# Optimization experiments

Hardware: AMD Instinct MI355X
Metric: run time of the kernel (lower is better)

Reference implementation:

```python
import jax, jax.numpy as jnp
import numpy as np

B, S, D = 4, 512, 512
H = 8
HD = D // H  # 64
F = 5  # num membership functions
EPS = 1e-8


def setup_inputs() -> dict:
    key = jax.random.key(0)
    ks = jax.random.split(key, 8)
    inp = {
        "x": jax.random.normal(ks[0], (B, S, D), jnp.float32),
        # linear projections (stored so that y = x @ W + b)
        "Wq": jax.random.normal(ks[1], (D, D), jnp.float32) / np.sqrt(D),
        "bq": jnp.zeros((D,), jnp.float32),
        "Wk": jax.random.normal(ks[2], (D, D), jnp.float32) / np.sqrt(D),
        "bk": jnp.zeros((D,), jnp.float32),
        "Wv": jax.random.normal(ks[3], (D, D), jnp.float32) / np.sqrt(D),
        "bv": jnp.zeros((D,), jnp.float32),
        "Wo": jax.random.normal(ks[4], (D, D), jnp.float32) / np.sqrt(D),
        "bo": jnp.zeros((D,), jnp.float32),
        # Gaussian membership params (init per nn.Parameter defaults)
        "g_centers": jax.random.normal(ks[5], (F, HD), jnp.float32),
        "g_sigmas": jnp.ones((F, HD), jnp.float32),
        "g_weights": jnp.ones((F,), jnp.float32),
        # learnable t-norm mixing logits
        "tnorm_weights": jnp.ones((3,), jnp.float32),
    }
    return inp


def _gaussian_membership(z, centers, sigmas, weights):
    # z: [B,H,S,HD] -> membership [B,H,S,F]
    nd = (z[..., None, :] - centers) / (sigmas + EPS)  # [B,H,S,F,HD]
    # prod_k exp(-0.5 nd_k^2) == exp(sum_k -0.5 nd_k^2)
    mem = jnp.exp(jnp.sum(-0.5 * nd * nd, axis=-1))  # [B,H,S,F]
    return mem * weights


def reference(x, Wq, bq, Wk, bk, Wv, bv, Wo, bo,
              g_centers, g_sigmas, g_weights, tnorm_weights):
    b, s, d = x.shape
    q = (x @ Wq + bq).reshape(b, s, H, HD).transpose(0, 2, 1, 3)  # [B,H,S,HD]
    k = (x @ Wk + bk).reshape(b, s, H, HD).transpose(0, 2, 1, 3)
    v = (x @ Wv + bv).reshape(b, s, H, HD).transpose(0, 2, 1, 3)

    qm = _gaussian_membership(q, g_centers, g_sigmas, g_weights)  # [B,H,S,F]
    km = _gaussian_membership(k, g_centers, g_sigmas, g_weights)  # [B,H,S,F]

    w = jax.nn.softmax(tnorm_weights)
    # product t-norm summed over F is a plain contraction
    prod_term = jnp.einsum('bhif,bhjf->bhij', qm, km)
    qe = qm[:, :, :, None, :]  # [B,H,S,1,F]
    ke = km[:, :, None, :, :]  # [B,H,1,S,F]
    min_term = jnp.sum(jnp.minimum(qe, ke), axis=-1)           # [B,H,S,S]
    luk_term = jnp.sum(jnp.maximum(qe + ke - 1.0, 0.0), axis=-1)
    scores = w[0] * prod_term + w[1] * min_term + w[2] * luk_term
    attn = jax.nn.softmax(scores, axis=-1)  # [B,H,S,S]

    out = jnp.einsum('bhij,bhjd->bhid', attn, v)  # [B,H,S,HD]
    out = out.transpose(0, 2, 1, 3).reshape(b, s, d)
    out = out @ Wo + bo  # dropout is identity in eval mode
    return out, attn
```

## Files before the change

kernel.cpp:

```cpp
#include <hip/hip_runtime.h>
#include <hip/hip_bf16.h>

#define B_  4
#define S_  512
#define D_  512
#define H_  8
#define HD_ 64
#define F_  5
#define NROW (B_*S_)
#define BHS  (B_*H_*S_)
#define EPS_ 1e-8f

typedef __attribute__((ext_vector_type(8))) short bf16x8;
typedef __attribute__((ext_vector_type(4))) float f32x4;

static __device__ __forceinline__ short f2bf(float f) {
    __hip_bfloat16 h = __float2bfloat16(f);
    return *reinterpret_cast<short*>(&h);
}

#define GLOAD16(ldsp, gp) \
    __builtin_amdgcn_global_load_lds( \
        (const __attribute__((address_space(1))) unsigned int*)(gp), \
        (__attribute__((address_space(3))) unsigned int*)(ldsp), 16, 0, 0)

__global__ __launch_bounds__(256) void convert_fused(
    const float* __restrict__ x,
    const float* __restrict__ Wq, const float* __restrict__ Wk,
    const float* __restrict__ Wv, const float* __restrict__ Wo,
    short* __restrict__ xb, short* __restrict__ WqkvT, short* __restrict__ WoT)
{
    const int bid = blockIdx.x;
    if (bid < 1024) {
        int i = bid * 256 + threadIdx.x;
        float4 f = reinterpret_cast<const float4*>(x)[i];
        short4 o;
        o.x = f2bf(f.x); o.y = f2bf(f.y); o.z = f2bf(f.z); o.w = f2bf(f.w);
        reinterpret_cast<short4*>(xb)[i] = o;
        return;
    }
    const int wb = bid - 1024;
    const int widx = wb >> 6;
    const int tile = wb & 63;
    const int k0 = (tile >> 3) * 64, n0 = (tile & 7) * 64;
    const float* __restrict__ src = widx==0?Wq:(widx==1?Wk:(widx==2?Wv:Wo));
    short* __restrict__ dst = (widx < 3) ? WqkvT : WoT;
    const int drow0 = (widx < 3) ? widx * 512 : 0;

    __shared__ short T[64][72];
    const int t = threadIdx.x;
    const int r = t >> 2, qq = t & 3;
#pragma unroll
    for (int i = 0; i < 4; ++i) {
        float4 f = *reinterpret_cast<const float4*>(&src[(k0+r)*D_ + n0 + qq*16 + i*4]);
        T[r][qq*16+i*4+0] = f2bf(f.x);
        T[r][qq*16+i*4+1] = f2bf(f.y);
        T[r][qq*16+i*4+2] = f2bf(f.z);
        T[r][qq*16+i*4+3] = f2bf(f.w);
    }
    __syncthreads();
    const int c = t >> 2;
#pragma unroll
    for (int i = 0; i < 4; ++i) {
        short4 o;
        o.x = T[qq*16+i*4+0][c];
        o.y = T[qq*16+i*4+1][c];
        o.z = T[qq*16+i*4+2][c];
        o.w = T[qq*16+i*4+3][c];
        *reinterpret_cast<short4*>(&dst[(size_t)(drow0+n0+c)*512 + k0 + qq*16 + i*4]) = o;
    }
}

__global__ __launch_bounds__(256) void qkv_mfma(
    const short* __restrict__ Ab, const short* __restrict__ BT,
    const float* __restrict__ bq, const float* __restrict__ bk,
    const float* __restrict__ bv,
    const float* __restrict__ gc, const float* __restrict__ gs,
    const float* __restrict__ gw,
    float* __restrict__ qm, float* __restrict__ km, short* __restrict__ vT)
{
    __shared__ short As[64*64];
    __shared__ short Bs[128*64];
    const int tid = threadIdx.x;
    const int wid = tid >> 6, lane = tid & 63;
    const int wr = wid >> 1, wc = wid & 1;
    const int m0 = blockIdx.x * 64, n0 = blockIdx.y * 128;

    f32x4 acc[2][4] = {};

    for (int k0 = 0; k0 < 512; k0 += 64) {
#pragma unroll
        for (int i = 0; i < 2; ++i) {
            const int c = wid*2 + i;
            const int row = c*8 + (lane >> 3);
            const int kk  = (lane & 7) * 8;
            GLOAD16(&As[c*512], &Ab[(size_t)(m0+row)*512 + k0 + kk]);
        }
#pragma unroll
        for (int i = 0; i < 4; ++i) {
            const int c = wid*4 + i;
            const int row = c*8 + (lane >> 3);
            const int kk  = (lane & 7) * 8;
            GLOAD16(&Bs[c*512], &BT[(size_t)(n0+row)*512 + k0 + kk]);
        }
        asm volatile("s_waitcnt vmcnt(0)" ::: "memory");
        __syncthreads();
#pragma unroll
        for (int ks = 0; ks < 2; ++ks) {
            bf16x8 a[2], b[4];
#pragma unroll
            for (int f = 0; f < 2; ++f) {
                const int ar = wr*32 + f*16 + (lane & 15);
                a[f] = *reinterpret_cast<const bf16x8*>(&As[ar*64 + ks*32 + (lane>>4)*8]);
            }
#pragma unroll
            for (int f = 0; f < 4; ++f) {
                const int br = wc*64 + f*16 + (lane & 15);
                b[f] = *reinterpret_cast<const bf16x8*>(&Bs[br*64 + ks*32 + (lane>>4)*8]);
            }
#pragma unroll
            for (int i = 0; i < 2; ++i)
#pragma unroll
                for (int j = 0; j < 4; ++j)
                    acc[i][j] = __builtin_amdgcn_mfma_f32_16x16x32_bf16(a[i], b[j], acc[i][j], 0, 0, 0);
        }
        __syncthreads();
    }

    const int wsel = n0 >> 9;
    const int h = ((n0 & 511) >> 6) + wc;
    const int b_ = m0 >> 9;
    const int bh = b_*H_ + h;
    const int hdl = lane & 15;

    if (wsel < 2) {
        const float* __restrict__ bias = wsel==0 ? bq : bk;
        float* __restrict__ dst        = wsel==0 ? qm : km;
        float gcv[F_][4], isv[F_][4], bi4[4];
#pragma unroll
        for (int f = 0; f < F_; ++f)
#pragma unroll
            for (int j = 0; j < 4; ++j) {
                const int hd = j*16 + hdl;
                gcv[f][j] = gc[f*HD_ + hd];
                isv[f][j] = 1.0f / (gs[f*HD_ + hd] + EPS_);
            }
#pragma unroll
        for (int j = 0; j < 4; ++j) bi4[j] = bias[h*64 + j*16 + hdl];
        float gwv[F_];
#pragma unroll
        for (int f = 0; f < F_; ++f) gwv[f] = gw[f];

#pragma unroll
        for (int i = 0; i < 2; ++i)
#pragma unroll
            for (int r = 0; r < 4; ++r) {
                float z[4];
#pragma unroll
                for (int j = 0; j < 4; ++j) z[j] = acc[i][j][r] + bi4[j];
                float p[F_];
#pragma unroll
                for (int f = 0; f < F_; ++f) {
                    float t = 0.f;
#pragma unroll
                    for (int j = 0; j < 4; ++j) {
                        const float nd = (z[j] - gcv[f][j]) * isv[f][j];
                        t = fmaf(nd*nd, -0.5f, t);
                    }
                    p[f] = t;
                }
#pragma unroll
                for (int off = 1; off < 16; off <<= 1)
#pragma unroll
                    for (int f = 0; f < F_; ++f) p[f] += __shfl_xor(p[f], off, 64);
                if (hdl == 0) {
                    const int m = m0 + wr*32 + i*16 + (lane>>4)*4 + r;
                    const int s = m & 511;
                    float* o = &dst[((size_t)bh*S_ + s)*F_];
#pragma unroll
                    for (int f = 0; f < F_; ++f) o[f] = expf(p[f]) * gwv[f];
                }
            }
    } else {
        float bi4[4];
#pragma unroll
        for (int j = 0; j < 4; ++j) bi4[j] = bv[h*64 + j*16 + hdl];
#pragma unroll
        for (int i = 0; i < 2; ++i)
#pragma unroll
            for (int j = 0; j < 4; ++j) {
                short4 o;
                o.x = f2bf(acc[i][j][0] + bi4[j]);
                o.y = f2bf(acc[i][j][1] + bi4[j]);
                o.z = f2bf(acc[i][j][2] + bi4[j]);
                o.w = f2bf(acc[i][j][3] + bi4[j]);
                const int sb = (m0 & 511) + wr*32 + i*16 + (lane>>4)*4;
                *reinterpret_cast<short4*>(
                    &vT[((size_t)bh*HD_ + j*16 + hdl)*S_ + sb]) = o;
            }
    }
}

__global__ __launch_bounds__(256) void scores_av(
    const float* __restrict__ qm, const float* __restrict__ km,
    const float* __restrict__ tw, const short* __restrict__ vT,
    float* __restrict__ attn, short* __restrict__ ctxb)
{
    __shared__ float qs[32*F_];
    __shared__ short P[32*512];
    const int s0 = blockIdx.x * 32;
    const int bh = blockIdx.y;
    const int tid = threadIdx.x, w = tid >> 6, lane = tid & 63;

    const float t0 = tw[0], t1 = tw[1], t2 = tw[2];
    const float mx3 = fmaxf(t0, fmaxf(t1, t2));
    const float e0 = __expf(t0-mx3), e1 = __expf(t1-mx3), e2 = __expf(t2-mx3);
    const float inv3 = 1.0f / (e0+e1+e2);
    const float w0 = e0*inv3, w1 = e1*inv3, w2 = e2*inv3;

    if (tid < 32*F_) qs[tid] = qm[((size_t)bh*S_ + s0)*F_ + tid];

    float kr[8][F_];
#pragma unroll
    for (int jj = 0; jj < 8; ++jj) {
        const size_t kb = ((size_t)bh*S_ + jj*64 + lane)*F_;
#pragma unroll
        for (int f = 0; f < F_; ++f) kr[jj][f] = km[kb + f];
    }
    __syncthreads();

#pragma unroll 2
    for (int rl = 0; rl < 8; ++rl) {
        const int i = w*8 + rl;
        const float q0 = qs[i*F_+0], q1 = qs[i*F_+1], q2 = qs[i*F_+2],
                    q3 = qs[i*F_+3], q4 = qs[i*F_+4];
        float s[8];
        float m = -INFINITY;
#pragma unroll
        for (int jj = 0; jj < 8; ++jj) {
            const float *kk = kr[jj];
            float prod = q0*kk[0] + q1*kk[1] + q2*kk[2] + q3*kk[3] + q4*kk[4];
            float mn = fminf(q0,kk[0]) + fminf(q1,kk[1]) + fminf(q2,kk[2])
                     + fminf(q3,kk[3]) + fminf(q4,kk[4]);
            float lk = fmaxf(q0+kk[0]-1.f,0.f) + fmaxf(q1+kk[1]-1.f,0.f)
                     + fmaxf(q2+kk[2]-1.f,0.f) + fmaxf(q3+kk[3]-1.f,0.f)
                     + fmaxf(q4+kk[4]-1.f,0.f);
            s[jj] = w0*prod + w1*mn + w2*lk;
            m = fmaxf(m, s[jj]);
        }
#pragma unroll
        for (int off = 32; off > 0; off >>= 1) m = fmaxf(m, __shfl_xor(m, off, 64));
        float e[8], sum = 0.f;
#pragma unroll
        for (int jj = 0; jj < 8; ++jj) { e[jj] = __expf(s[jj]-m); sum += e[jj]; }
#pragma unroll
        for (int off = 32; off > 0; off >>= 1) sum += __shfl_xor(sum, off, 64);
        const float invs = 1.0f / sum;
#pragma unroll
        for (int jj = 0; jj < 8; ++jj) {
            const float a = e[jj]*invs;
            attn[((size_t)(bh*S_ + s0 + i))*S_ + jj*64 + lane] = a;
            const int byte = i*1024 + (jj*64 + lane)*2;
            *reinterpret_cast<short*>(
                reinterpret_cast<char*>(P) + (byte ^ ((i&7)<<4))) = f2bf(a);
        }
    }
    __syncthreads();

    const short* __restrict__ Vb = vT + (size_t)bh*HD_*S_;
    const int h0 = (w & 1) * 16;
    const int f0 = (w >> 1) * 2;
    f32x4 acc[2] = {};
    const int arow = h0 + (lane & 15);
    const int asw  = (arow & 7) << 4;
#pragma unroll
    for (int ks = 0; ks < 16; ++ks) {
        const int abyte = arow*1024 + ks*64 + (lane>>4)*16;
        const bf16x8 a = *reinterpret_cast<const bf16x8*>(
            reinterpret_cast<const char*>(P) + (abyte ^ asw));
#pragma unroll
        for (int ff = 0; ff < 2; ++ff) {
            const bf16x8 b = *reinterpret_cast<const bf16x8*>(
                &Vb[(size_t)((f0+ff)*16 + (lane & 15))*S_ + ks*32 + (lane>>4)*8]);
            acc[ff] = __builtin_amdgcn_mfma_f32_16x16x32_bf16(a, b, acc[ff], 0, 0, 0);
        }
    }
    const int b_ = bh >> 3, h = bh & 7;
#pragma unroll
    for (int ff = 0; ff < 2; ++ff)
#pragma unroll
        for (int r = 0; r < 4; ++r) {
            const int s = s0 + h0 + (lane>>4)*4 + r;
            ctxb[((size_t)(b_*S_ + s))*D_ + h*HD_ + (f0+ff)*16 + (lane & 15)]
                = f2bf(acc[ff][r]);
        }
}

__global__ __launch_bounds__(256) void out_mfma(
    const short* __restrict__ ctxb, const short* __restrict__ WoT,
    const float* __restrict__ bo, float* __restrict__ out)
{
    const int m0 = blockIdx.x * 64;
    const int n0 = blockIdx.y * 64;

    __shared__ short As[64*64];
    __shared__ short Bs[64*64];
    const int tid = threadIdx.x;
    const int wid = tid >> 6, lane = tid & 63;
    const int wr = wid >> 1, wc = wid & 1;

    f32x4 acc[2][2] = {};

    for (int k0 = 0; k0 < D_; k0 += 64) {
#pragma unroll
        for (int i = 0; i < 2; ++i) {
            const int c = wid*2 + i;
            const int row = c*8 + (lane >> 3);
            const int kk  = (lane & 7) * 8;
            GLOAD16(&As[c*512], &ctxb[(size_t)(m0+row)*D_ + k0 + kk]);
            GLOAD16(&Bs[c*512], &WoT[(size_t)(n0+row)*D_ + k0 + kk]);
        }
        asm volatile("s_waitcnt vmcnt(0)" ::: "memory");
        __syncthreads();
#pragma unroll
        for (int ks = 0; ks < 2; ++ks) {
            bf16x8 a[2], b[2];
#pragma unroll
            for (int f = 0; f < 2; ++f) {
                const int ar = wr*32 + f*16 + (lane & 15);
                a[f] = *reinterpret_cast<const bf16x8*>(&As[ar*64 + ks*32 + (lane>>4)*8]);
                const int br = wc*32 + f*16 + (lane & 15);
                b[f] = *reinterpret_cast<const bf16x8*>(&Bs[br*64 + ks*32 + (lane>>4)*8]);
            }
#pragma unroll
            for (int i = 0; i < 2; ++i)
#pragma unroll
                for (int j = 0; j < 2; ++j)
                    acc[i][j] = __builtin_amdgcn_mfma_f32_16x16x32_bf16(a[i], b[j], acc[i][j], 0, 0, 0);
        }
        __syncthreads();
    }
#pragma unroll
    for (int i = 0; i < 2; ++i)
#pragma unroll
        for (int j = 0; j < 2; ++j)
#pragma unroll
            for (int r = 0; r < 4; ++r) {
                const int m = m0 + wr*32 + i*16 + (lane>>4)*4 + r;
                const int n = n0 + wc*32 + j*16 + (lane & 15);
                out[(size_t)m*D_ + n] = acc[i][j][r] + bo[n];
            }
}

extern "C" void kernel_launch(void* const* d_in, const int* in_sizes, int n_in,
                              void* d_out, int out_size, void* d_ws, size_t ws_size,
                              hipStream_t stream)
{
    const float* x  = (const float*)d_in[0];
    const float* Wq = (const float*)d_in[1];
    const float* bq = (const float*)d_in[2];
    const float* Wk = (const float*)d_in[3];
    const float* bk = (const float*)d_in[4];
    const float* Wv = (const float*)d_in[5];
    const float* bv = (const float*)d_in[6];
    const float* Wo = (const float*)d_in[7];
    const float* bo = (const float*)d_in[8];
    const float* gc = (const float*)d_in[9];
    const float* gs = (const float*)d_in[10];
    const float* gw = (const float*)d_in[11];
    const float* tw = (const float*)d_in[12];

    short* xb    = (short*)d_ws;
    short* WqkvT = xb + 1048576;
    short* WoT   = WqkvT + 786432;
    short* vT    = WoT + 262144;
    short* ctxb  = vT + 1048576;
    float* qm    = (float*)(ctxb + 1048576);
    float* km    = qm + 81920;

    float* out0 = (float*)d_out;
    float* attn = out0 + (size_t)B_*S_*D_;

    convert_fused<<<1280, 256, 0, stream>>>(x, Wq, Wk, Wv, Wo, xb, WqkvT, WoT);
    qkv_mfma<<<dim3(NROW/64, 1536/128), 256, 0, stream>>>(
        xb, WqkvT, bq, bk, bv, gc, gs, gw, qm, km, vT);
    scores_av<<<dim3(S_/32, B_*H_), 256, 0, stream>>>(qm, km, tw, vT, attn, ctxb);
    out_mfma<<<dim3(NROW/64, D_/64), 256, 0, stream>>>(ctxb, WoT, bo, out0);
}
```

Baseline: 55.33 us.

## Double-buffer GEMM LDS tiles and vectorize attention key loads and stores

Both GEMM kernels (QKV and output projection) now double-buffer their LDS tiles, so the global-to-LDS load of the next K slice is issued before the MFMAs on the current one, overlapping memory latency with compute. The attention kernel remaps keys so each lane owns 8 contiguous keys. This lets key memberships load as float4 vectors, the fp32 attention rows be written with two 16-byte nontemporal stores, and the bf16 P tile be written as one packed 16-byte LDS store. The cost is twice the LDS in the GEMMs, which may lower occupancy, and a different, strided lane-to-key ordering.

```diff
diff --git a/kernel.cpp b/kernel.cpp
--- a/kernel.cpp
+++ b/kernel.cpp
@@ -79,8 +79,8 @@
     const float* __restrict__ gw,
     float* __restrict__ qm, float* __restrict__ km, short* __restrict__ vT)
 {
-    __shared__ short As[64*64];
-    __shared__ short Bs[128*64];
+    __shared__ short As[2][64*64];
+    __shared__ short Bs[2][128*64];
     const int tid = threadIdx.x;
     const int wid = tid >> 6, lane = tid & 63;
     const int wr = wid >> 1, wc = wid & 1;
@@ -88,35 +88,42 @@
 
     f32x4 acc[2][4] = {};
 
-    for (int k0 = 0; k0 < 512; k0 += 64) {
+    const int srow = lane >> 3;
+    const int skk  = (lane & 7) * 8;
+
+    auto stage = [&](int buf, int k0) {
 #pragma unroll
         for (int i = 0; i < 2; ++i) {
             const int c = wid*2 + i;
-            const int row = c*8 + (lane >> 3);
-            const int kk  = (lane & 7) * 8;
-            GLOAD16(&As[c*512], &Ab[(size_t)(m0+row)*512 + k0 + kk]);
+            GLOAD16(&As[buf][c*512], &Ab[(size_t)(m0 + c*8 + srow)*512 + k0 + skk]);
         }
 #pragma unroll
         for (int i = 0; i < 4; ++i) {
             const int c = wid*4 + i;
-            const int row = c*8 + (lane >> 3);
-            const int kk  = (lane & 7) * 8;
-            GLOAD16(&Bs[c*512], &BT[(size_t)(n0+row)*512 + k0 + kk]);
-        }
-        asm volatile("s_waitcnt vmcnt(0)" ::: "memory");
-        __syncthreads();
+            GLOAD16(&Bs[buf][c*512], &BT[(size_t)(n0 + c*8 + srow)*512 + k0 + skk]);
+        }
+    };
+
+    stage(0, 0);
+    asm volatile("s_waitcnt vmcnt(0)" ::: "memory");
+    __syncthreads();
+
+#pragma unroll
+    for (int t = 0; t < 8; ++t) {
+        const int cur = t & 1;
+        if (t < 7) stage(cur ^ 1, (t+1)*64);
 #pragma unroll
         for (int ks = 0; ks < 2; ++ks) {
             bf16x8 a[2], b[4];
 #pragma unroll
             for (int f = 0; f < 2; ++f) {
                 const int ar = wr*32 + f*16 + (lane & 15);
-                a[f] = *reinterpret_cast<const bf16x8*>(&As[ar*64 + ks*32 + (lane>>4)*8]);
+                a[f] = *reinterpret_cast<const bf16x8*>(&As[cur][ar*64 + ks*32 + (lane>>4)*8]);
             }
 #pragma unroll
             for (int f = 0; f < 4; ++f) {
                 const int br = wc*64 + f*16 + (lane & 15);
-                b[f] = *reinterpret_cast<const bf16x8*>(&Bs[br*64 + ks*32 + (lane>>4)*8]);
+                b[f] = *reinterpret_cast<const bf16x8*>(&Bs[cur][br*64 + ks*32 + (lane>>4)*8]);
             }
 #pragma unroll
             for (int i = 0; i < 2; ++i)
@@ -124,6 +131,7 @@
                 for (int j = 0; j < 4; ++j)
                     acc[i][j] = __builtin_amdgcn_mfma_f32_16x16x32_bf16(a[i], b[j], acc[i][j], 0, 0, 0);
         }
+        asm volatile("s_waitcnt vmcnt(0)" ::: "memory");
         __syncthreads();
     }
 
@@ -220,12 +228,13 @@
 
     if (tid < 32*F_) qs[tid] = qm[((size_t)bh*S_ + s0)*F_ + tid];
 
-    float kr[8][F_];
-#pragma unroll
-    for (int jj = 0; jj < 8; ++jj) {
-        const size_t kb = ((size_t)bh*S_ + jj*64 + lane)*F_;
-#pragma unroll
-        for (int f = 0; f < F_; ++f) kr[jj][f] = km[kb + f];
+    float krf[40];
+    {
+        const float4* kmp = reinterpret_cast<const float4*>(
+            &km[(size_t)bh*S_*F_ + lane*40]);
+#pragma unroll
+        for (int u = 0; u < 10; ++u)
+            reinterpret_cast<float4*>(krf)[u] = kmp[u];
     }
     __syncthreads();
 
@@ -238,7 +247,7 @@
         float m = -INFINITY;
 #pragma unroll
         for (int jj = 0; jj < 8; ++jj) {
-            const float *kk = kr[jj];
+            const float *kk = &krf[jj*F_];
             float prod = q0*kk[0] + q1*kk[1] + q2*kk[2] + q3*kk[3] + q4*kk[4];
             float mn = fminf(q0,kk[0]) + fminf(q1,kk[1]) + fminf(q2,kk[2])
                      + fminf(q3,kk[3]) + fminf(q4,kk[4]);
@@ -256,14 +265,20 @@
 #pragma unroll
         for (int off = 32; off > 0; off >>= 1) sum += __shfl_xor(sum, off, 64);
         const float invs = 1.0f / sum;
-#pragma unroll
-        for (int jj = 0; jj < 8; ++jj) {
-            const float a = e[jj]*invs;
-            attn[((size_t)(bh*S_ + s0 + i))*S_ + jj*64 + lane] = a;
-            const int byte = i*1024 + (jj*64 + lane)*2;
-            *reinterpret_cast<short*>(
-                reinterpret_cast<char*>(P) + (byte ^ ((i&7)<<4))) = f2bf(a);
-        }
+
+        float a[8];
+#pragma unroll
+        for (int jj = 0; jj < 8; ++jj) a[jj] = e[jj]*invs;
+        float* arow = &attn[((size_t)(bh*S_ + s0 + i))*S_ + lane*8];
+        f32x4 v0 = { a[0], a[1], a[2], a[3] };
+        f32x4 v1 = { a[4], a[5], a[6], a[7] };
+        __builtin_nontemporal_store(v0, reinterpret_cast<f32x4*>(arow));
+        __builtin_nontemporal_store(v1, reinterpret_cast<f32x4*>(arow) + 1);
+        bf16x8 pk;
+#pragma unroll
+        for (int jj = 0; jj < 8; ++jj) pk[jj] = f2bf(a[jj]);
+        *reinterpret_cast<bf16x8*>(
+            reinterpret_cast<char*>(P) + ((i*1024 + lane*16) ^ ((i&7)<<4))) = pk;
     }
     __syncthreads();
 
@@ -303,34 +318,43 @@
     const int m0 = blockIdx.x * 64;
     const int n0 = blockIdx.y * 64;
 
-    __shared__ short As[64*64];
-    __shared__ short Bs[64*64];
+    __shared__ short As[2][64*64];
+    __shared__ short Bs[2][64*64];
     const int tid = threadIdx.x;
     const int wid = tid >> 6, lane = tid & 63;
     const int wr = wid >> 1, wc = wid & 1;
 
     f32x4 acc[2][2] = {};
 
-    for (int k0 = 0; k0 < D_; k0 += 64) {
+    const int srow = lane >> 3;
+    const int skk  = (lane & 7) * 8;
+
+    auto stage = [&](int buf, int k0) {
 #pragma unroll
         for (int i = 0; i < 2; ++i) {
             const int c = wid*2 + i;
-            const int row = c*8 + (lane >> 3);
-            const int kk  = (lane & 7) * 8;
-            GLOAD16(&As[c*512], &ctxb[(size_t)(m0+row)*D_ + k0 + kk]);
-            GLOAD16(&Bs[c*512], &WoT[(size_t)(n0+row)*D_ + k0 + kk]);
-        }
-        asm volatile("s_waitcnt vmcnt(0)" ::: "memory");
-        __syncthreads();
+            GLOAD16(&As[buf][c*512], &ctxb[(size_t)(m0 + c*8 + srow)*D_ + k0 + skk]);
+            GLOAD16(&Bs[buf][c*512], &WoT[(size_t)(n0 + c*8 + srow)*D_ + k0 + skk]);
+        }
+    };
+
+    stage(0, 0);
+    asm volatile("s_waitcnt vmcnt(0)" ::: "memory");
+    __syncthreads();
+
+#pragma unroll
+    for (int t = 0; t < 8; ++t) {
+        const int cur = t & 1;
+        if (t < 7) stage(cur ^ 1, (t+1)*64);
 #pragma unroll
         for (int ks = 0; ks < 2; ++ks) {
             bf16x8 a[2], b[2];
 #pragma unroll
             for (int f = 0; f < 2; ++f) {
                 const int ar = wr*32 + f*16 + (lane & 15);
-                a[f] = *reinterpret_cast<const bf16x8*>(&As[ar*64 + ks*32 + (lane>>4)*8]);
+                a[f] = *reinterpret_cast<const bf16x8*>(&As[cur][ar*64 + ks*32 + (lane>>4)*8]);
                 const int br = wc*32 + f*16 + (lane & 15);
-                b[f] = *reinterpret_cast<const bf16x8*>(&Bs[br*64 + ks*32 + (lane>>4)*8]);
+                b[f] = *reinterpret_cast<const bf16x8*>(&Bs[cur][br*64 + ks*32 + (lane>>4)*8]);
             }
 #pragma unroll
             for (int i = 0; i < 2; ++i)
@@ -338,6 +362,7 @@
                 for (int j = 0; j < 2; ++j)
                     acc[i][j] = __builtin_amdgcn_mfma_f32_16x16x32_bf16(a[i], b[j], acc[i][j], 0, 0, 0);
         }
+        asm volatile("s_waitcnt vmcnt(0)" ::: "memory");
         __syncthreads();
     }
 #pragma unroll
```

Result: slower. 57.77 us (+4.4%).

## Remap key columns per lane to vectorize km loads and attn/P stores

Applied to the files above, without the earlier changes.

Each lane now owns 8 contiguous key columns (lane*8..lane*8+7) instead of a stride-64 pattern. The per-lane key memberships then come in as ten float4 loads, each attention row is written as two 16-byte nontemporal stores, and the bf16 probabilities go to LDS as one 16-byte write. The goal is fewer and wider global and LDS transactions, plus less cache pollution from the large attn output. The score loop and the P layout stay consistent because softmax is order-independent. The float4 cast of km assumes 16-byte alignment, which holds since bh*S*F*4 and lane*160 are multiples of 16.

```diff
diff --git a/kernel.cpp b/kernel.cpp
--- a/kernel.cpp
+++ b/kernel.cpp
@@ -220,12 +220,13 @@
 
     if (tid < 32*F_) qs[tid] = qm[((size_t)bh*S_ + s0)*F_ + tid];
 
-    float kr[8][F_];
-#pragma unroll
-    for (int jj = 0; jj < 8; ++jj) {
-        const size_t kb = ((size_t)bh*S_ + jj*64 + lane)*F_;
-#pragma unroll
-        for (int f = 0; f < F_; ++f) kr[jj][f] = km[kb + f];
+    float krf[40];
+    {
+        const float4* kmp = reinterpret_cast<const float4*>(
+            &km[(size_t)bh*S_*F_ + lane*40]);
+#pragma unroll
+        for (int u = 0; u < 10; ++u)
+            reinterpret_cast<float4*>(krf)[u] = kmp[u];
     }
     __syncthreads();
 
@@ -238,7 +239,7 @@
         float m = -INFINITY;
 #pragma unroll
         for (int jj = 0; jj < 8; ++jj) {
-            const float *kk = kr[jj];
+            const float *kk = &krf[jj*F_];
             float prod = q0*kk[0] + q1*kk[1] + q2*kk[2] + q3*kk[3] + q4*kk[4];
             float mn = fminf(q0,kk[0]) + fminf(q1,kk[1]) + fminf(q2,kk[2])
                      + fminf(q3,kk[3]) + fminf(q4,kk[4]);
@@ -256,14 +257,20 @@
 #pragma unroll
         for (int off = 32; off > 0; off >>= 1) sum += __shfl_xor(sum, off, 64);
         const float invs = 1.0f / sum;
-#pragma unroll
-        for (int jj = 0; jj < 8; ++jj) {
-            const float a = e[jj]*invs;
-            attn[((size_t)(bh*S_ + s0 + i))*S_ + jj*64 + lane] = a;
-            const int byte = i*1024 + (jj*64 + lane)*2;
-            *reinterpret_cast<short*>(
-                reinterpret_cast<char*>(P) + (byte ^ ((i&7)<<4))) = f2bf(a);
-        }
+
+        float a[8];
+#pragma unroll
+        for (int jj = 0; jj < 8; ++jj) a[jj] = e[jj]*invs;
+        float* arow = &attn[((size_t)(bh*S_ + s0 + i))*S_ + lane*8];
+        f32x4 v0 = { a[0], a[1], a[2], a[3] };
+        f32x4 v1 = { a[4], a[5], a[6], a[7] };
+        __builtin_nontemporal_store(v0, reinterpret_cast<f32x4*>(arow));
+        __builtin_nontemporal_store(v1, reinterpret_cast<f32x4*>(arow) + 1);
+        bf16x8 pk;
+#pragma unroll
+        for (int jj = 0; jj < 8; ++jj) pk[jj] = f2bf(a[jj]);
+        *reinterpret_cast<bf16x8*>(
+            reinterpret_cast<char*>(P) + ((i*1024 + lane*16) ^ ((i&7)<<4))) = pk;
     }
     __syncthreads();
 
```

New measurement: 54.96 us. About the same (-0.7%).
